# Performance work log

Measured on AMD Instinct MI355X. Metric: run time of the kernel, lower is better.

The kernel has to match this reference:

```python
import jax, jax.numpy as jnp
import numpy as np

EPS_MSG = 1e-7   # GENConv message epsilon
BN_EPS = 1e-5    # BatchNorm1d eps
NUM_GRAPHS = 1024


def _linear(x, W, b):
    return x @ W + b


def _batchnorm(x, gamma, beta):
    # training-mode batch statistics over the node dimension
    mu = jnp.mean(x, axis=0)
    var = jnp.mean((x - mu) ** 2, axis=0)
    return (x - mu) * jax.lax.rsqrt(var + BN_EPS) * gamma + beta


def _genconv(x, src, dst, e, t, W1, b1, gamma, beta, W2, b2, num_nodes):
    # message: relu(x_j + edge_attr) + eps, shape [E, H]
    msg = jax.nn.relu(x[src] + e) + EPS_MSG
    # learnable softmax aggregation over each destination's neighborhood
    s = msg * t
    m = jax.lax.stop_gradient(jax.ops.segment_max(s, dst, num_segments=num_nodes))
    m = jnp.where(jnp.isfinite(m), m, 0.0)
    ex = jnp.exp(s - m[dst])
    denom = jax.ops.segment_sum(ex, dst, num_segments=num_nodes)
    alpha = ex / (denom[dst] + 1e-16)
    agg = jax.ops.segment_sum(msg * alpha, dst, num_segments=num_nodes)  # [N, H]
    # GENConv MLP([H, 2H, H], norm='batch') applied to x + aggregated messages
    h = x + agg
    h = _linear(h, W1, b1)
    h = _batchnorm(h, gamma, beta)
    h = jax.nn.relu(h)
    return _linear(h, W2, b2)


def setup_inputs() -> dict:
    key = jax.random.key(0)
    N, E, FIN, FE, H, L, G, OUT = 50000, 1000000, 32, 16, 64, 4, NUM_GRAPHS, 1
    ks = jax.random.split(key, 32)

    def rn(k, shape, fan_in):
        return jax.random.normal(k, shape, dtype=jnp.float32) * (1.0 / np.sqrt(fan_in))

    inp = {}
    inp["x"] = jax.random.normal(ks[0], (N, FIN), dtype=jnp.float32)
    inp["edge_attr"] = jax.random.normal(ks[1], (E, FE), dtype=jnp.float32)
    inp["edge_index"] = jax.random.randint(ks[2], (2, E), 0, N)
    inp["batch"] = jnp.sort(jax.random.randint(ks[3], (N,), 0, G))
    # atom encoder: Linear(FIN,H) ReLU Linear(H,H) ReLU
    inp["atom_W1"] = rn(ks[4], (FIN, H), FIN); inp["atom_b1"] = jnp.zeros((H,), jnp.float32)
    inp["atom_W2"] = rn(ks[5], (H, H), H);     inp["atom_b2"] = jnp.zeros((H,), jnp.float32)
    # bond encoder: Linear(FE,H) ReLU Linear(H,H) ReLU
    inp["bond_W1"] = rn(ks[6], (FE, H), FE);   inp["bond_b1"] = jnp.zeros((H,), jnp.float32)
    inp["bond_W2"] = rn(ks[7], (H, H), H);     inp["bond_b2"] = jnp.zeros((H,), jnp.float32)
    # stacked GENConv params (L layers)
    inp["conv_t"] = jnp.ones((L,), jnp.float32)
    inp["conv_W1"] = rn(ks[8], (L, H, 2 * H), H)
    inp["conv_b1"] = jnp.zeros((L, 2 * H), jnp.float32)
    inp["conv_gamma"] = jnp.ones((L, 2 * H), jnp.float32)
    inp["conv_beta"] = jnp.zeros((L, 2 * H), jnp.float32)
    inp["conv_W2"] = rn(ks[9], (L, 2 * H, H), 2 * H)
    inp["conv_b2"] = jnp.zeros((L, H), jnp.float32)
    # head
    inp["lin1_W"] = rn(ks[10], (H, H), H);     inp["lin1_b"] = jnp.zeros((H,), jnp.float32)
    inp["lin2_W"] = rn(ks[11], (H, OUT), H);   inp["lin2_b"] = jnp.zeros((OUT,), jnp.float32)
    return inp


def reference(x, edge_attr, atom_W1, atom_b1, atom_W2, atom_b2,
              bond_W1, bond_b1, bond_W2, bond_b2,
              conv_t, conv_W1, conv_b1, conv_gamma, conv_beta, conv_W2, conv_b2,
              lin1_W, lin1_b, lin2_W, lin2_b,
              edge_index, batch):
    N = x.shape[0]
    src, dst = edge_index[0], edge_index[1]
    h = jax.nn.relu(_linear(jax.nn.relu(_linear(x, atom_W1, atom_b1)), atom_W2, atom_b2))
    e = jax.nn.relu(_linear(jax.nn.relu(_linear(edge_attr, bond_W1, bond_b1)), bond_W2, bond_b2))
    L = conv_t.shape[0]
    for i in range(L):
        h = _genconv(h, src, dst, e, conv_t[i], conv_W1[i], conv_b1[i],
                     conv_gamma[i], conv_beta[i], conv_W2[i], conv_b2[i], N)
        if i < L - 1:
            h = jax.nn.relu(h)
    g = jax.ops.segment_sum(h, batch, num_segments=NUM_GRAPHS)  # global_add_pool
    g = jax.nn.relu(_linear(g, lin1_W, lin1_b))
    return _linear(g, lin2_W, lin2_b)
```

## Files before the change

kernel.cpp:

```cpp
#include <hip/hip_runtime.h>
#include <hip/hip_bf16.h>
#include <math.h>

typedef __attribute__((ext_vector_type(8))) short bf16x8;
typedef __attribute__((ext_vector_type(4))) float f32x4;

__device__ inline unsigned f2bf(float f) {
    union { __hip_bfloat16 h; unsigned short u; } cv;
    cv.h = __float2bfloat16(f);
    return (unsigned)cv.u;
}
__device__ inline float bfu(unsigned u) {
    return __uint_as_float(u << 16);
}


__global__ void k_hist(const int* __restrict__ dst, int* __restrict__ counts, int E) {
    int e = blockIdx.x * blockDim.x + threadIdx.x;
    if (e < E) atomicAdd(&counts[dst[e]], 1);
}

__global__ void k_scan1(const int* __restrict__ counts, int* __restrict__ row_ptr,
                        int* __restrict__ csum, int n) {
    __shared__ int buf[1024];
    int tid = threadIdx.x;
    int base = blockIdx.x * 1024;
    int v = (base + tid < n) ? counts[base + tid] : 0;
    buf[tid] = v;
    __syncthreads();
    int inc = v;
    for (int off = 1; off < 1024; off <<= 1) {
        int add = (tid >= off) ? buf[tid - off] : 0;
        __syncthreads();
        inc += add;
        buf[tid] = inc;
        __syncthreads();
    }
    if (base + tid < n) row_ptr[base + tid] = inc - v;
    if (tid == 1023) csum[blockIdx.x] = inc;
}

__global__ void k_scan2(int* __restrict__ csum, int nc, int* __restrict__ total) {
    if (threadIdx.x == 0) {
        int run = 0;
        for (int i = 0; i < nc; ++i) { int c = csum[i]; csum[i] = run; run += c; }
        *total = run;
    }
}

__global__ void k_scan3(int* __restrict__ row_ptr, const int* __restrict__ csum,
                        const int* __restrict__ total, int n) {
    int i = blockIdx.x * blockDim.x + threadIdx.x;
    if (i < n) row_ptr[i] += csum[i >> 10];
    if (i == 0) row_ptr[n] = *total;
}

#define ECH 4096
__global__ __launch_bounds__(256) void k_scatter(const int* __restrict__ src,
                          const int* __restrict__ dst,
                          const int* __restrict__ row_ptr, int* __restrict__ fill,
                          int2* __restrict__ spe, int E, int NS) {
    int bs = blockIdx.x & 7;
    int chunk = blockIdx.x >> 3;
    int base = chunk * ECH;
    int lo = bs * NS, hi = lo + NS;
#pragma unroll 1
    for (int j = 0; j < ECH / 256; ++j) {
        int e = base + j * 256 + threadIdx.x;
        if (e < E) {
            int d = dst[e];
            if (d >= lo && d < hi) {
                int pos = row_ptr[d] + atomicAdd(&fill[d], 1);
                spe[pos] = make_int2(src[e], e);
            }
        }
    }
}

__global__ void k_gptr(const int* __restrict__ batch, int* __restrict__ gptr, int n, int G) {
    int i = blockIdx.x * blockDim.x + threadIdx.x;
    if (i > n) return;
    if (i == 0) {
        int b0 = batch[0];
        for (int g = 0; g <= b0; ++g) gptr[g] = 0;
    } else if (i == n) {
        int bl = batch[n - 1];
        for (int g = bl + 1; g <= G; ++g) gptr[g] = n;
    } else {
        int b = batch[i], pb = batch[i - 1];
        for (int g = pb + 1; g <= b; ++g) gptr[g] = i;
    }
}


__global__ void k_wt(const float* __restrict__ W1, const float* __restrict__ W2,
                     unsigned short* __restrict__ W1b, unsigned short* __restrict__ W2tb) {
    int tid = blockIdx.x * blockDim.x + threadIdx.x;
    if (tid < 1024) {
        int j = tid / 16, k = tid % 16;
        W1b[j * 16 + k] = (unsigned short)f2bf(W1[k * 64 + j]);
    }
    if (tid < 4096) {
        int j = tid / 64, k = tid % 64;
        W2tb[j * 64 + k] = (unsigned short)f2bf(W2[k * 64 + j]);
    }
}

__global__ void k_wtc(const float* __restrict__ W1, const float* __restrict__ W2,
                      unsigned short* __restrict__ W1tb, unsigned short* __restrict__ W2tb,
                      int L) {
    int idx = blockIdx.x * blockDim.x + threadIdx.x;
    int tot = L * 8192;
    if (idx < tot) {
        int l = idx / 8192, r = idx % 8192;
        int j = r / 64, k = r % 64;
        W1tb[(long)l * 8192 + j * 64 + k] = (unsigned short)f2bf(W1[(long)l * 8192 + k * 128 + j]);
        int j2 = r / 128, k2 = r % 128;
        W2tb[(long)l * 8192 + j2 * 128 + k2] =
            (unsigned short)f2bf(W2[(long)l * 8192 + k2 * 64 + j2]);
    }
}


#define TM 128
__global__ __launch_bounds__(256) void k_atom(const float* __restrict__ x,
        const float* __restrict__ W1, const float* __restrict__ b1,
        const float* __restrict__ W2, const float* __restrict__ b2,
        float* __restrict__ out, unsigned short* __restrict__ hb, int M) {
    __shared__ float sU[TM * 65];
    __shared__ float sW1[32 * 64];
    __shared__ float sW2[64 * 64];
    __shared__ float sB1[64], sB2[64];
#define A_IN(r, c) sU[(r) * 33 + (c)]
#define A_T1(r, c) sU[(r) * 65 + (c)]
    int tid = threadIdx.x;
    int base = blockIdx.x * TM;
    for (int i = tid; i < 32 * 64 / 4; i += 256) ((float4*)sW1)[i] = ((const float4*)W1)[i];
    for (int i = tid; i < 64 * 64 / 4; i += 256) ((float4*)sW2)[i] = ((const float4*)W2)[i];
    if (tid < 64) { sB1[tid] = b1[tid]; sB2[tid] = b2[tid]; }
    for (int i = tid; i < TM * 32 / 4; i += 256) {
        int r = i / 8, c4 = i % 8;
        int row = base + r;
        float4 v = (row < M) ? ((const float4*)(x + (long)row * 32))[c4] : make_float4(0, 0, 0, 0);
        A_IN(r, c4 * 4 + 0) = v.x; A_IN(r, c4 * 4 + 1) = v.y;
        A_IN(r, c4 * 4 + 2) = v.z; A_IN(r, c4 * 4 + 3) = v.w;
    }
    __syncthreads();
    int r0 = (tid / 16) * 8;
    int c0 = (tid % 16) * 4;
    float acc[8][4];
#pragma unroll
    for (int i = 0; i < 8; i++)
#pragma unroll
        for (int j = 0; j < 4; j++) acc[i][j] = sB1[c0 + j];
    for (int k = 0; k < 32; k++) {
        float a[8], b[4];
#pragma unroll
        for (int i = 0; i < 8; i++) a[i] = A_IN(r0 + i, k);
#pragma unroll
        for (int j = 0; j < 4; j++) b[j] = sW1[k * 64 + c0 + j];
#pragma unroll
        for (int i = 0; i < 8; i++)
#pragma unroll
            for (int j = 0; j < 4; j++) acc[i][j] += a[i] * b[j];
    }
    __syncthreads();
#pragma unroll
    for (int i = 0; i < 8; i++)
#pragma unroll
        for (int j = 0; j < 4; j++) A_T1(r0 + i, c0 + j) = fmaxf(acc[i][j], 0.f);
    __syncthreads();
#pragma unroll
    for (int i = 0; i < 8; i++)
#pragma unroll
        for (int j = 0; j < 4; j++) acc[i][j] = sB2[c0 + j];
    for (int k = 0; k < 64; k++) {
        float a[8], b[4];
#pragma unroll
        for (int i = 0; i < 8; i++) a[i] = A_T1(r0 + i, k);
#pragma unroll
        for (int j = 0; j < 4; j++) b[j] = sW2[k * 64 + c0 + j];
#pragma unroll
        for (int i = 0; i < 8; i++)
#pragma unroll
            for (int j = 0; j < 4; j++) acc[i][j] += a[i] * b[j];
    }
#pragma unroll
    for (int i = 0; i < 8; i++) {
        int row = base + r0 + i;
        if (row < M) {
            float4 v = make_float4(fmaxf(acc[i][0], 0.f), fmaxf(acc[i][1], 0.f),
                                   fmaxf(acc[i][2], 0.f), fmaxf(acc[i][3], 0.f));
            *(float4*)(out + (long)row * 64 + c0) = v;
            unsigned p01 = f2bf(v.x) | (f2bf(v.y) << 16);
            unsigned p23 = f2bf(v.z) | (f2bf(v.w) << 16);
            *(uint2*)(hb + (long)row * 64 + c0) = make_uint2(p01, p23);
        }
    }
}


__global__ __launch_bounds__(256) void k_bond(const float* __restrict__ ea,
        const int2* __restrict__ spe,
        const unsigned short* __restrict__ W1b, const float* __restrict__ b1,
        const unsigned short* __restrict__ W2tb, const float* __restrict__ b2,
        unsigned short* __restrict__ e_q, int E) {
    __shared__ unsigned sT1[128 * 32];
    __shared__ unsigned sW2[64 * 32];
    int tid = threadIdx.x;

    for (int i = tid; i < 2048; i += 256) {
        int rw = i >> 5, cp = i & 31;
        sW2[rw * 32 + (cp ^ ((rw & 7) << 2))] = ((const unsigned*)W2tb)[i];
    }

    int wv = tid >> 6, lane = tid & 63;
    int lr = lane & 15, q = lane >> 4;

    union { bf16x8 v; uint4 u4; } bf1[4];
    float bias1[4];
#pragma unroll
    for (int nt = 0; nt < 4; ++nt) {
        bf1[nt].u4 = make_uint4(0, 0, 0, 0);
        if (q < 2)
            bf1[nt].u4 = *(const uint4*)(W1b + (nt * 16 + lr) * 16 + q * 8);
        bias1[nt] = b1[nt * 16 + lr];
    }

#pragma unroll
    for (int mt1 = 0; mt1 < 2; ++mt1) {
        int rtile = wv * 2 + mt1;
        long row1 = (long)blockIdx.x * 128 + rtile * 16 + lr;
        long eidx = row1 < (long)E ? row1 : (long)(E - 1);
        int eid = spe[eidx].y;
        union { bf16x8 v; uint4 u4; unsigned u[4]; } af1;
        af1.u4 = make_uint4(0, 0, 0, 0);
        if (q < 2) {
            const float4* er = (const float4*)(ea + (long)eid * 16 + q * 8);
            float4 u0 = er[0], u1 = er[1];
            af1.u[0] = f2bf(u0.x) | (f2bf(u0.y) << 16);
            af1.u[1] = f2bf(u0.z) | (f2bf(u0.w) << 16);
            af1.u[2] = f2bf(u1.x) | (f2bf(u1.y) << 16);
            af1.u[3] = f2bf(u1.z) | (f2bf(u1.w) << 16);
        }
#pragma unroll
        for (int nt = 0; nt < 4; ++nt) {
            f32x4 c0;
            c0[0] = bias1[nt]; c0[1] = bias1[nt]; c0[2] = bias1[nt]; c0[3] = bias1[nt];
            f32x4 d = __builtin_amdgcn_mfma_f32_16x16x32_bf16(af1.v, bf1[nt].v, c0, 0, 0, 0);
#pragma unroll
            for (int i = 0; i < 4; ++i) {
                unsigned hv = f2bf(fmaxf(d[i], 0.f));
                unsigned ov = (unsigned)__shfl_xor((int)hv, 1, 64);
                if ((lr & 1) == 0) {
                    int r = rtile * 16 + q * 4 + i;
                    int cp = nt * 8 + (lr >> 1);
                    sT1[r * 32 + (cp ^ ((r & 7) << 2))] = hv | (ov << 16);
                }
            }
        }
    }
    __syncthreads();

    bf16x8 bf[4][2];
#pragma unroll
    for (int nt = 0; nt < 4; ++nt)
#pragma unroll
        for (int ks = 0; ks < 2; ++ks) {
            int rw = nt * 16 + lr;
            int u = rw * 32 + ((ks * 16 + q * 4) ^ ((rw & 7) << 2));
            bf[nt][ks] = *(const bf16x8*)&sW2[u];
        }
    f32x4 acc[2][4];
#pragma unroll
    for (int mt = 0; mt < 2; ++mt)
#pragma unroll
        for (int nt = 0; nt < 4; ++nt) {
            float bias = b2[nt * 16 + lr];
            f32x4 c0; c0[0] = bias; c0[1] = bias; c0[2] = bias; c0[3] = bias;
            acc[mt][nt] = c0;
        }
#pragma unroll
    for (int mt = 0; mt < 2; ++mt) {
        int rw = (wv * 2 + mt) * 16 + lr;
#pragma unroll
        for (int ks = 0; ks < 2; ++ks) {
            int u = rw * 32 + ((ks * 16 + q * 4) ^ ((rw & 7) << 2));
            bf16x8 af = *(const bf16x8*)&sT1[u];
#pragma unroll
            for (int nt = 0; nt < 4; ++nt)
                acc[mt][nt] = __builtin_amdgcn_mfma_f32_16x16x32_bf16(
                    af, bf[nt][ks], acc[mt][nt], 0, 0, 0);
        }
    }
#pragma unroll
    for (int mt = 0; mt < 2; ++mt)
#pragma unroll
        for (int nt = 0; nt < 4; ++nt) {
            long r0 = (long)blockIdx.x * 128 + (wv * 2 + mt) * 16 + q * 4;
            unsigned p01 = f2bf(fmaxf(acc[mt][nt][0], 0.f)) |
                           (f2bf(fmaxf(acc[mt][nt][1], 0.f)) << 16);
            unsigned p23 = f2bf(fmaxf(acc[mt][nt][2], 0.f)) |
                           (f2bf(fmaxf(acc[mt][nt][3], 0.f)) << 16);
            long qb = ((r0 >> 2) * 64 + nt * 16 + lr) * 4;
            if (r0 + 3 < (long)E) {
                *(uint2*)(e_q + qb) = make_uint2(p01, p23);
            } else {
                unsigned vv[4] = {p01 & 0xffff, p01 >> 16, p23 & 0xffff, p23 >> 16};
#pragma unroll
                for (int i = 0; i < 4; ++i)
                    if (r0 + i < (long)E) e_q[qb + i] = (unsigned short)vv[i];
            }
        }
}


__global__ __launch_bounds__(256) void k_agg(const float* __restrict__ h,
        const unsigned short* __restrict__ h_bf,
        const unsigned short* __restrict__ e_q, const int2* __restrict__ spe,
        const int* __restrict__ row_ptr, const float* __restrict__ t_ptr, int layer,
        unsigned short* __restrict__ yb, int n) {
    int wid = blockIdx.x * 4 + (threadIdx.x >> 6);
    int lane = threadIdx.x & 63;
    if (wid >= n) return;
    wid = __builtin_amdgcn_readfirstlane(wid);
    float tval = t_ptr[layer];
    int beg = row_ptr[wid], end = row_ptr[wid + 1];
    float m = -INFINITY, den = 0.f, num = 0.f;
    int i = beg;
    int astart = (beg + 3) & ~3; if (astart > end) astart = end;
    int aend = end & ~3;         if (aend < astart) aend = astart;
    for (; i < astart; ++i) {
        int s = spe[i].x;
        float ev = bfu((unsigned)e_q[((long)(i >> 2) * 64 + lane) * 4 + (i & 3)]);
        float hv = bfu((unsigned)h_bf[(long)s * 64 + lane]);
        float msg = fmaxf(hv + ev, 0.f) + 1e-7f;
        float sv = msg * tval;
        float mn = fmaxf(m, sv);
        float sc = __expf(m - mn);
        float w = __expf(sv - mn);
        den = den * sc + w;
        num = num * sc + w * msg;
        m = mn;
    }
    for (; i + 8 <= aend; i += 8) {
        int s0 = spe[i].x,     s1 = spe[i + 1].x, s2 = spe[i + 2].x, s3 = spe[i + 3].x;
        int s4 = spe[i + 4].x, s5 = spe[i + 5].x, s6 = spe[i + 6].x, s7 = spe[i + 7].x;
        uint2 ea0 = *(const uint2*)(e_q + ((long)(i >> 2) * 64 + lane) * 4);
        uint2 ea1 = *(const uint2*)(e_q + ((long)((i >> 2) + 1) * 64 + lane) * 4);
        float hv0 = bfu((unsigned)h_bf[(long)s0 * 64 + lane]);
        float hv1 = bfu((unsigned)h_bf[(long)s1 * 64 + lane]);
        float hv2 = bfu((unsigned)h_bf[(long)s2 * 64 + lane]);
        float hv3 = bfu((unsigned)h_bf[(long)s3 * 64 + lane]);
        float hv4 = bfu((unsigned)h_bf[(long)s4 * 64 + lane]);
        float hv5 = bfu((unsigned)h_bf[(long)s5 * 64 + lane]);
        float hv6 = bfu((unsigned)h_bf[(long)s6 * 64 + lane]);
        float hv7 = bfu((unsigned)h_bf[(long)s7 * 64 + lane]);
        float msg0 = fmaxf(hv0 + bfu(ea0.x & 0xffff), 0.f) + 1e-7f;
        float msg1 = fmaxf(hv1 + bfu(ea0.x >> 16), 0.f) + 1e-7f;
        float msg2 = fmaxf(hv2 + bfu(ea0.y & 0xffff), 0.f) + 1e-7f;
        float msg3 = fmaxf(hv3 + bfu(ea0.y >> 16), 0.f) + 1e-7f;
        float msg4 = fmaxf(hv4 + bfu(ea1.x & 0xffff), 0.f) + 1e-7f;
        float msg5 = fmaxf(hv5 + bfu(ea1.x >> 16), 0.f) + 1e-7f;
        float msg6 = fmaxf(hv6 + bfu(ea1.y & 0xffff), 0.f) + 1e-7f;
        float msg7 = fmaxf(hv7 + bfu(ea1.y >> 16), 0.f) + 1e-7f;
        float sv0 = msg0 * tval, sv1 = msg1 * tval, sv2 = msg2 * tval, sv3 = msg3 * tval;
        float sv4 = msg4 * tval, sv5 = msg5 * tval, sv6 = msg6 * tval, sv7 = msg7 * tval;
        float mn = fmaxf(fmaxf(fmaxf(fmaxf(m, sv0), fmaxf(sv1, sv2)),
                               fmaxf(fmaxf(sv3, sv4), fmaxf(sv5, sv6))), sv7);
        float sc = __expf(m - mn);
        float w0 = __expf(sv0 - mn), w1 = __expf(sv1 - mn);
        float w2 = __expf(sv2 - mn), w3 = __expf(sv3 - mn);
        float w4 = __expf(sv4 - mn), w5 = __expf(sv5 - mn);
        float w6 = __expf(sv6 - mn), w7 = __expf(sv7 - mn);
        den = den * sc + (((w0 + w1) + (w2 + w3)) + ((w4 + w5) + (w6 + w7)));
        num = num * sc + (((w0 * msg0 + w1 * msg1) + (w2 * msg2 + w3 * msg3)) +
                          ((w4 * msg4 + w5 * msg5) + (w6 * msg6 + w7 * msg7)));
        m = mn;
    }
    for (; i < aend; i += 4) {
        int s0 = spe[i].x, s1 = spe[i + 1].x, s2 = spe[i + 2].x, s3 = spe[i + 3].x;
        uint2 ee = *(const uint2*)(e_q + ((long)(i >> 2) * 64 + lane) * 4);
        float hv0 = bfu((unsigned)h_bf[(long)s0 * 64 + lane]);
        float hv1 = bfu((unsigned)h_bf[(long)s1 * 64 + lane]);
        float hv2 = bfu((unsigned)h_bf[(long)s2 * 64 + lane]);
        float hv3 = bfu((unsigned)h_bf[(long)s3 * 64 + lane]);
        float msg0 = fmaxf(hv0 + bfu(ee.x & 0xffff), 0.f) + 1e-7f;
        float msg1 = fmaxf(hv1 + bfu(ee.x >> 16), 0.f) + 1e-7f;
        float msg2 = fmaxf(hv2 + bfu(ee.y & 0xffff), 0.f) + 1e-7f;
        float msg3 = fmaxf(hv3 + bfu(ee.y >> 16), 0.f) + 1e-7f;
        float sv0 = msg0 * tval, sv1 = msg1 * tval;
        float sv2 = msg2 * tval, sv3 = msg3 * tval;
        float mn = fmaxf(fmaxf(fmaxf(m, sv0), fmaxf(sv1, sv2)), sv3);
        float sc = __expf(m - mn);
        float w0 = __expf(sv0 - mn);
        float w1 = __expf(sv1 - mn);
        float w2 = __expf(sv2 - mn);
        float w3 = __expf(sv3 - mn);
        den = den * sc + ((w0 + w1) + (w2 + w3));
        num = num * sc + ((w0 * msg0 + w1 * msg1) + (w2 * msg2 + w3 * msg3));
        m = mn;
    }
    for (; i < end; ++i) {
        int s = spe[i].x;
        float ev = bfu((unsigned)e_q[((long)(i >> 2) * 64 + lane) * 4 + (i & 3)]);
        float hv = bfu((unsigned)h_bf[(long)s * 64 + lane]);
        float msg = fmaxf(hv + ev, 0.f) + 1e-7f;
        float sv = msg * tval;
        float mn = fmaxf(m, sv);
        float sc = __expf(m - mn);
        float w = __expf(sv - mn);
        den = den * sc + w;
        num = num * sc + w * msg;
        m = mn;
    }
    float agg = (end > beg) ? num / (den + 1e-16f) : 0.f;
    yb[(long)wid * 64 + lane] = (unsigned short)f2bf(h[(long)wid * 64 + lane] + agg);
}


__global__ __launch_bounds__(256) void k_gemm1(const unsigned* __restrict__ yb,
        const unsigned* __restrict__ W1tb, const float* __restrict__ b1,
        unsigned* __restrict__ h1b, float* __restrict__ part, int n) {
    __shared__ unsigned sY[128 * 32];
    __shared__ unsigned sW[128 * 32];
    int tid = threadIdx.x;
    int base = blockIdx.x * 128;
    for (int i = tid; i < 4096; i += 256) {
        int rw = i >> 5, cp = i & 31;
        sW[rw * 32 + (cp ^ ((rw & 7) << 2))] = W1tb[i];
    }
#pragma unroll
    for (int j = 0; j < 16; ++j) {
        int u = j * 256 + tid;
        int r = u >> 5, cp = u & 31;
        long row = base + r;
        unsigned v = (row < (long)n) ? yb[row * 32 + cp] : 0u;
        sY[r * 32 + (cp ^ ((r & 7) << 2))] = v;
    }
    __syncthreads();
    int wv = tid >> 6, lane = tid & 63, lr = lane & 15, q = lane >> 4;
    bf16x8 bf[2][2];
    float bias[2];
#pragma unroll
    for (int nt2 = 0; nt2 < 2; ++nt2) {
        int rw = wv * 32 + nt2 * 16 + lr;
#pragma unroll
        for (int ks = 0; ks < 2; ++ks)
            bf[nt2][ks] = *(const bf16x8*)&sW[rw * 32 + ((ks * 16 + q * 4) ^ ((rw & 7) << 2))];
        bias[nt2] = b1[rw];
    }
    float ps[2] = {0, 0}, ps2[2] = {0, 0};
#pragma unroll 1
    for (int mt = 0; mt < 8; ++mt) {
        int ar = mt * 16 + lr;
        bf16x8 a0 = *(const bf16x8*)&sY[ar * 32 + ((q * 4) ^ ((ar & 7) << 2))];
        bf16x8 a1 = *(const bf16x8*)&sY[ar * 32 + ((16 + q * 4) ^ ((ar & 7) << 2))];
#pragma unroll
        for (int nt2 = 0; nt2 < 2; ++nt2) {
            f32x4 acc;
            acc[0] = bias[nt2]; acc[1] = bias[nt2]; acc[2] = bias[nt2]; acc[3] = bias[nt2];
            acc = __builtin_amdgcn_mfma_f32_16x16x32_bf16(a0, bf[nt2][0], acc, 0, 0, 0);
            acc = __builtin_amdgcn_mfma_f32_16x16x32_bf16(a1, bf[nt2][1], acc, 0, 0, 0);
            int col = wv * 32 + nt2 * 16 + lr;
#pragma unroll
            for (int i = 0; i < 4; ++i) {
                long row = base + mt * 16 + q * 4 + i;
                float v = acc[i];
                unsigned hv = f2bf(v);
                unsigned ov = (unsigned)__shfl_xor((int)hv, 1, 64);
                bool in = row < (long)n;
                if (in) { ps[nt2] += v; ps2[nt2] += v * v; }
                if (in && (lr & 1) == 0)
                    h1b[row * 64 + ((unsigned)col >> 1)] = hv | (ov << 16);
            }
        }
    }
#pragma unroll
    for (int nt2 = 0; nt2 < 2; ++nt2) {
        float s = ps[nt2], s2 = ps2[nt2];
        s += __shfl_down(s, 32, 64);  s += __shfl_down(s, 16, 64);
        s2 += __shfl_down(s2, 32, 64); s2 += __shfl_down(s2, 16, 64);
        if (lane < 16) {
            int col = wv * 32 + nt2 * 16 + lr;
            part[(long)blockIdx.x * 256 + col] = s;
            part[(long)blockIdx.x * 256 + 128 + col] = s2;
        }
    }
}


__global__ __launch_bounds__(256) void k_bnred(const float* __restrict__ part,
                                               float* __restrict__ part2, int nblk) {
    int c = threadIdx.x;
    int b = blockIdx.x;
    float s = 0.f;
    for (int r = b; r < nblk; r += 64) s += part[(long)r * 256 + c];
    part2[b * 256 + c] = s;
}

__global__ __launch_bounds__(1024) void k_bnfin(const float* __restrict__ part2,
                        const float* __restrict__ gamma, const float* __restrict__ beta,
                        float* __restrict__ scale, float* __restrict__ shift, float invN) {
    __shared__ float red[4][256];
    __shared__ float tot[256];
    int c = threadIdx.x & 255;
    int g = threadIdx.x >> 8;
    float s = 0.f;
#pragma unroll
    for (int r = 0; r < 16; ++r) s += part2[(g * 16 + r) * 256 + c];
    red[g][c] = s;
    __syncthreads();
    if (threadIdx.x < 256) tot[c] = red[0][c] + red[1][c] + red[2][c] + red[3][c];
    __syncthreads();
    if (threadIdx.x < 128) {
        int cc = threadIdx.x;
        float mu = tot[cc] * invN;
        float var = fmaxf(tot[128 + cc] * invN - mu * mu, 0.f);
        float sc = gamma[cc] * rsqrtf(var + 1e-5f);
        scale[cc] = sc;
        shift[cc] = beta[cc] - mu * sc;
    }
}


__global__ __launch_bounds__(256) void k_gemm2(const unsigned* __restrict__ h1b,
        const float* __restrict__ scale, const float* __restrict__ shift,
        const unsigned* __restrict__ W2tbL, const float* __restrict__ b2,
        float* __restrict__ hout, unsigned short* __restrict__ hb, int n, int dorelu) {
    __shared__ unsigned sA[128 * 64];
    __shared__ unsigned sW[64 * 64];
    __shared__ float sSc[128], sSh[128];
    int tid = threadIdx.x;
    int base = blockIdx.x * 128;
    if (tid < 128) { sSc[tid] = scale[tid]; sSh[tid] = shift[tid]; }
    for (int i = tid; i < 4096; i += 256) {
        int rw = i >> 6, cp = i & 63;
        sW[rw * 64 + (cp ^ ((rw & 7) << 2))] = W2tbL[i];
    }
    __syncthreads();
#pragma unroll
    for (int j = 0; j < 32; ++j) {
        int u = j * 256 + tid;
        int r = u >> 6, cp = u & 63;
        long row = base + r;
        unsigned w = 0;
        if (row < (long)n) {
            unsigned hv = h1b[row * 64 + cp];
            float v0 = fmaxf(bfu(hv & 0xffff) * sSc[2 * cp] + sSh[2 * cp], 0.f);
            float v1 = fmaxf(bfu(hv >> 16) * sSc[2 * cp + 1] + sSh[2 * cp + 1], 0.f);
            w = f2bf(v0) | (f2bf(v1) << 16);
        }
        sA[r * 64 + (cp ^ ((r & 7) << 2))] = w;
    }
    __syncthreads();
    int wv = tid >> 6, lane = tid & 63, lr = lane & 15, q = lane >> 4;
    bf16x8 bf[4];
    {
        int rw = wv * 16 + lr;
#pragma unroll
        for (int ks = 0; ks < 4; ++ks)
            bf[ks] = *(const bf16x8*)&sW[rw * 64 + ((ks * 16 + q * 4) ^ ((rw & 7) << 2))];
    }
    float bias = b2[wv * 16 + lr];
#pragma unroll 1
    for (int mt = 0; mt < 8; ++mt) {
        int ar = mt * 16 + lr;
        f32x4 acc;
        acc[0] = bias; acc[1] = bias; acc[2] = bias; acc[3] = bias;
#pragma unroll
        for (int ks = 0; ks < 4; ++ks) {
            bf16x8 a = *(const bf16x8*)&sA[ar * 64 + ((ks * 16 + q * 4) ^ ((ar & 7) << 2))];
            acc = __builtin_amdgcn_mfma_f32_16x16x32_bf16(a, bf[ks], acc, 0, 0, 0);
        }
        int col = wv * 16 + lr;
#pragma unroll
        for (int i = 0; i < 4; ++i) {
            long row = base + mt * 16 + q * 4 + i;
            float v = dorelu ? fmaxf(acc[i], 0.f) : acc[i];
            unsigned hv = f2bf(v);
            unsigned ov = (unsigned)__shfl_xor((int)hv, 1, 64);
            if (row < (long)n) {
                hout[row * 64 + col] = v;
                if (dorelu && (lr & 1) == 0)
                    *(unsigned*)(hb + row * 64 + (col & ~1)) = hv | (ov << 16);
            }
        }
    }
}


__global__ __launch_bounds__(64) void k_head(const float* __restrict__ h,
        const int* __restrict__ gptr,
        const float* __restrict__ W1, const float* __restrict__ b1,
        const float* __restrict__ W2, const float* __restrict__ b2,
        float* __restrict__ out) {
    int g = blockIdx.x;
    int lane = threadIdx.x;
    int beg = gptr[g], end = gptr[g + 1];
    float s = 0.f;
    for (int r = beg; r < end; ++r) s += h[(long)r * 64 + lane];
    __shared__ float sg[64];
    sg[lane] = s;
    __syncthreads();
    float acc = b1[lane];
    for (int k = 0; k < 64; k++) acc += sg[k] * W1[k * 64 + lane];
    acc = fmaxf(acc, 0.f);
    float v = acc * W2[lane];
#pragma unroll
    for (int off = 32; off > 0; off >>= 1) v += __shfl_down(v, off, 64);
    if (lane == 0) out[g] = v + b2[0];
}


extern "C" void kernel_launch(void* const* d_in, const int* in_sizes, int n_in,
                              void* d_out, int out_size, void* d_ws, size_t ws_size,
                              hipStream_t stream) {
    const float* x      = (const float*)d_in[0];
    const float* ea     = (const float*)d_in[1];
    const int*   ei     = (const int*)d_in[2];
    const int*   batch  = (const int*)d_in[3];
    const float* atomW1 = (const float*)d_in[4];
    const float* atomb1 = (const float*)d_in[5];
    const float* atomW2 = (const float*)d_in[6];
    const float* atomb2 = (const float*)d_in[7];
    const float* bondW1 = (const float*)d_in[8];
    const float* bondb1 = (const float*)d_in[9];
    const float* bondW2 = (const float*)d_in[10];
    const float* bondb2 = (const float*)d_in[11];
    const float* convT  = (const float*)d_in[12];
    const float* convW1 = (const float*)d_in[13];
    const float* convb1 = (const float*)d_in[14];
    const float* convG  = (const float*)d_in[15];
    const float* convBt = (const float*)d_in[16];
    const float* convW2 = (const float*)d_in[17];
    const float* convb2 = (const float*)d_in[18];
    const float* lin1W  = (const float*)d_in[19];
    const float* lin1b  = (const float*)d_in[20];
    const float* lin2W  = (const float*)d_in[21];
    const float* lin2b  = (const float*)d_in[22];
    float* out = (float*)d_out;

    const int N = in_sizes[0] / 32;
    const int E = in_sizes[1] / 16;
    const int G = out_size;
    const int Lconv = in_sizes[12];
    const int nchunk = (N + 1023) / 1024;
    const int nblk128 = (N + 127) / 128;
    const int NS = (N + 7) / 8;
    const int nchE = (E + ECH - 1) / ECH;
    const size_t nquad = (size_t)((E + 3) / 4);

    size_t need = 0;
    auto count = [&](size_t bytes) { need += (bytes + 255) & ~(size_t)255; };
    count(nquad * 4 * 64 * 2);
    count((size_t)N * 64 * 4);
    count((size_t)N * 64 * 2);
    count((size_t)N * 64 * 2);
    count((size_t)N * 128 * 2);
    count((size_t)E * 8);
    count((size_t)(N + 1) * 4);
    count((size_t)N * 4);
    count((size_t)N * 4);
    count((size_t)(G + 1) * 4);
    count((size_t)nblk128 * 256 * 4);
    count((size_t)64 * 256 * 4);
    count(128 * 4); count(128 * 4);
    count((size_t)(nchunk + 1) * 4);
    count(4);
    count(1024 * 2);
    count(4096 * 2);
    count((size_t)Lconv * 8192 * 2);
    count((size_t)Lconv * 8192 * 2);
    if (ws_size < need) {
        hipMemsetAsync(d_out, 0, (size_t)out_size * 4, stream);
        return;
    }

    char* ws = (char*)d_ws;
    size_t off = 0;
    auto alloc = [&](size_t bytes) -> void* {
        void* p = ws + off;
        off += (bytes + 255) & ~(size_t)255;
        return p;
    };
    unsigned short* e_q = (unsigned short*)alloc(nquad * 4 * 64 * 2);
    float* h_cur    = (float*)alloc((size_t)N * 64 * 4);
    unsigned short* h_bf = (unsigned short*)alloc((size_t)N * 64 * 2);
    unsigned short* y_bf = (unsigned short*)alloc((size_t)N * 64 * 2);
    unsigned short* h1b  = (unsigned short*)alloc((size_t)N * 128 * 2);
    int2*  spe      = (int2*)alloc((size_t)E * 8);
    int*   row_ptr  = (int*)alloc((size_t)(N + 1) * 4);
    int*   counts   = (int*)alloc((size_t)N * 4);
    int*   fill     = (int*)alloc((size_t)N * 4);
    int*   gptr     = (int*)alloc((size_t)(G + 1) * 4);
    float* part     = (float*)alloc((size_t)nblk128 * 256 * 4);
    float* part2    = (float*)alloc((size_t)64 * 256 * 4);
    float* bnscale  = (float*)alloc(128 * 4);
    float* bnshift  = (float*)alloc(128 * 4);
    int*   csum     = (int*)alloc((size_t)(nchunk + 1) * 4);
    int*   totalp   = (int*)alloc(4);
    unsigned short* W1b  = (unsigned short*)alloc(1024 * 2);
    unsigned short* W2tb = (unsigned short*)alloc(4096 * 2);
    unsigned short* cW1tb = (unsigned short*)alloc((size_t)Lconv * 8192 * 2);
    unsigned short* cW2tb = (unsigned short*)alloc((size_t)Lconv * 8192 * 2);
    (void)n_in;

    hipMemsetAsync(counts, 0, (size_t)N * 4, stream);
    hipMemsetAsync(fill, 0, (size_t)N * 4, stream);

    const int* src = ei;
    const int* dst = ei + E;

    k_hist<<<(E + 255) / 256, 256, 0, stream>>>(dst, counts, E);
    k_scan1<<<nchunk, 1024, 0, stream>>>(counts, row_ptr, csum, N);
    k_scan2<<<1, 64, 0, stream>>>(csum, nchunk, totalp);
    k_scan3<<<(N + 255) / 256, 256, 0, stream>>>(row_ptr, csum, totalp, N);
    k_scatter<<<nchE * 8, 256, 0, stream>>>(src, dst, row_ptr, fill, spe, E, NS);
    k_gptr<<<(N + 256) / 256, 256, 0, stream>>>(batch, gptr, N, G);
    k_wt<<<16, 256, 0, stream>>>(bondW1, bondW2, W1b, W2tb);
    k_wtc<<<(Lconv * 8192 + 255) / 256, 256, 0, stream>>>(convW1, convW2, cW1tb, cW2tb, Lconv);

    k_atom<<<(N + TM - 1) / TM, 256, 0, stream>>>(x, atomW1, atomb1, atomW2, atomb2,
                                                  h_cur, h_bf, N);
    k_bond<<<(E + 127) / 128, 256, 0, stream>>>(ea, spe, W1b, bondb1, W2tb, bondb2, e_q, E);

    for (int l = 0; l < Lconv; ++l) {
        k_agg<<<(N + 3) / 4, 256, 0, stream>>>(h_cur, h_bf, e_q, spe, row_ptr, convT, l,
                                               y_bf, N);
        k_gemm1<<<nblk128, 256, 0, stream>>>((const unsigned*)y_bf,
                                             (const unsigned*)(cW1tb + (size_t)l * 8192),
                                             convb1 + (size_t)l * 128,
                                             (unsigned*)h1b, part, N);
        k_bnred<<<64, 256, 0, stream>>>(part, part2, nblk128);
        k_bnfin<<<1, 1024, 0, stream>>>(part2, convG + (size_t)l * 128, convBt + (size_t)l * 128,
                                        bnscale, bnshift, 1.0f / (float)N);
        k_gemm2<<<nblk128, 256, 0, stream>>>((const unsigned*)h1b, bnscale, bnshift,
                                             (const unsigned*)(cW2tb + (size_t)l * 8192),
                                             convb2 + (size_t)l * 64, h_cur, h_bf, N,
                                             (l < Lconv - 1) ? 1 : 0);
    }

    k_head<<<G, 64, 0, stream>>>(h_cur, gptr, lin1W, lin1b, lin2W, lin2b, out);
}
```

Measured before the change: 535.1 us.

## Replace 8-pass CSR scatter with two-level bucket partition and swap MFMA operands in bond encoder

The CSR build previously scanned the whole edge list eight times, once per destination range. It now does a single pass that partitions edges into 64 destination buckets in a packed staging buffer, using block-local histograms and shared-memory atomics. A second kernel then scatters each bucket into its final CSR slots, so global atomics and writes stay within a localized range. Separately, the bond encoder's first MFMA has its operands swapped so each lane holds four consecutive columns for one row. Those can be packed straight into shared memory, which removes the shuffle and half-idle lanes. The cost is an extra E*8-byte staging buffer, one more kernel launch, and a packing scheme that needs src below 2^24 and a bucket size below 2^16.

```diff
diff --git a/kernel.cpp b/kernel.cpp
--- a/kernel.cpp
+++ b/kernel.cpp
@@ -55,25 +55,63 @@
     if (i == 0) row_ptr[n] = *total;
 }
 
-#define ECH 4096
-__global__ __launch_bounds__(256) void k_scatter(const int* __restrict__ src,
-                          const int* __restrict__ dst,
-                          const int* __restrict__ row_ptr, int* __restrict__ fill,
-                          int2* __restrict__ spe, int E, int NS) {
-    int bs = blockIdx.x & 7;
-    int chunk = blockIdx.x >> 3;
-    int base = chunk * ECH;
-    int lo = bs * NS, hi = lo + NS;
+
+#define ECH2 4096
+__global__ __launch_bounds__(256) void k_part(const int* __restrict__ src,
+        const int* __restrict__ dst, const int* __restrict__ row_ptr,
+        int* __restrict__ bfill, unsigned long long* __restrict__ staging,
+        int E, int NS64, int N) {
+    __shared__ int lh[64], lbase[64], lfill[64];
+    int tid = threadIdx.x;
+    if (tid < 64) lh[tid] = 0;
+    __syncthreads();
+    int base = blockIdx.x * ECH2;
 #pragma unroll 1
-    for (int j = 0; j < ECH / 256; ++j) {
-        int e = base + j * 256 + threadIdx.x;
+    for (int j = 0; j < ECH2 / 256; ++j) {
+        int e = base + j * 256 + tid;
+        if (e < E) atomicAdd(&lh[dst[e] / NS64], 1);
+    }
+    __syncthreads();
+    if (tid < 64) {
+        int bs = row_ptr[min(tid * NS64, N)];
+        lbase[tid] = bs + atomicAdd(&bfill[tid], lh[tid]);
+        lfill[tid] = 0;
+    }
+    __syncthreads();
+#pragma unroll 1
+    for (int j = 0; j < ECH2 / 256; ++j) {
+        int e = base + j * 256 + tid;
         if (e < E) {
             int d = dst[e];
-            if (d >= lo && d < hi) {
-                int pos = row_ptr[d] + atomicAdd(&fill[d], 1);
-                spe[pos] = make_int2(src[e], e);
-            }
-        }
+            int b = d / NS64;
+            int r = atomicAdd(&lfill[b], 1);
+            unsigned long long pk = (unsigned long long)((unsigned)src[e] & 0xffffffu)
+                | ((unsigned long long)((unsigned)(d - b * NS64) & 0xffffu) << 24)
+                | ((unsigned long long)(unsigned)e << 40);
+            staging[lbase[b] + r] = pk;
+        }
+    }
+}
+
+__global__ __launch_bounds__(256) void k_scat2(const unsigned long long* __restrict__ staging,
+        const int* __restrict__ row_ptr, int* __restrict__ fill,
+        int2* __restrict__ spe, int NS64, int N) {
+    int b = blockIdx.x >> 1;
+    int half = blockIdx.x & 1;
+    int s0 = row_ptr[min(b * NS64, N)];
+    int s1 = row_ptr[min((b + 1) * NS64, N)];
+    int cnt = s1 - s0;
+    int h0 = cnt >> 1;
+    int start = s0 + (half ? h0 : 0);
+    int len = half ? (cnt - h0) : h0;
+    for (int i = threadIdx.x; i < len; i += 256) {
+        unsigned long long pk = staging[start + i];
+        int srcv = (int)(pk & 0xffffffu);
+        int dloc = (int)((pk >> 24) & 0xffffu);
+        int eid  = (int)(pk >> 40);
+        int d = b * NS64 + dloc;
+        int pos = row_ptr[d] + atomicAdd(&fill[d], 1);
+        spe[pos] = make_int2(srcv, eid);
     }
 }
 
@@ -218,13 +256,13 @@
     int lr = lane & 15, q = lane >> 4;
 
     union { bf16x8 v; uint4 u4; } bf1[4];
-    float bias1[4];
+    float4 bias1[4];
 #pragma unroll
     for (int nt = 0; nt < 4; ++nt) {
         bf1[nt].u4 = make_uint4(0, 0, 0, 0);
         if (q < 2)
             bf1[nt].u4 = *(const uint4*)(W1b + (nt * 16 + lr) * 16 + q * 8);
-        bias1[nt] = b1[nt * 16 + lr];
+        bias1[nt] = *(const float4*)(b1 + nt * 16 + q * 4);
     }
 
 #pragma unroll
@@ -243,21 +281,18 @@
             af1.u[2] = f2bf(u1.x) | (f2bf(u1.y) << 16);
             af1.u[3] = f2bf(u1.z) | (f2bf(u1.w) << 16);
         }
+        int r = rtile * 16 + lr;
 #pragma unroll
         for (int nt = 0; nt < 4; ++nt) {
             f32x4 c0;
-            c0[0] = bias1[nt]; c0[1] = bias1[nt]; c0[2] = bias1[nt]; c0[3] = bias1[nt];
-            f32x4 d = __builtin_amdgcn_mfma_f32_16x16x32_bf16(af1.v, bf1[nt].v, c0, 0, 0, 0);
-#pragma unroll
-            for (int i = 0; i < 4; ++i) {
-                unsigned hv = f2bf(fmaxf(d[i], 0.f));
-                unsigned ov = (unsigned)__shfl_xor((int)hv, 1, 64);
-                if ((lr & 1) == 0) {
-                    int r = rtile * 16 + q * 4 + i;
-                    int cp = nt * 8 + (lr >> 1);
-                    sT1[r * 32 + (cp ^ ((r & 7) << 2))] = hv | (ov << 16);
-                }
-            }
+            c0[0] = bias1[nt].x; c0[1] = bias1[nt].y;
+            c0[2] = bias1[nt].z; c0[3] = bias1[nt].w;
+            f32x4 d = __builtin_amdgcn_mfma_f32_16x16x32_bf16(bf1[nt].v, af1.v, c0, 0, 0, 0);
+            unsigned p01 = f2bf(fmaxf(d[0], 0.f)) | (f2bf(fmaxf(d[1], 0.f)) << 16);
+            unsigned p23 = f2bf(fmaxf(d[2], 0.f)) | (f2bf(fmaxf(d[3], 0.f)) << 16);
+            int cp = nt * 8 + q * 2;
+            sT1[r * 32 + (cp ^ ((r & 7) << 2))] = p01;
+            sT1[r * 32 + ((cp + 1) ^ ((r & 7) << 2))] = p23;
         }
     }
     __syncthreads();
@@ -647,8 +682,8 @@
     const int Lconv = in_sizes[12];
     const int nchunk = (N + 1023) / 1024;
     const int nblk128 = (N + 127) / 128;
-    const int NS = (N + 7) / 8;
-    const int nchE = (E + ECH - 1) / ECH;
+    const int NS64 = (N + 63) / 64;
+    const int nchE2 = (E + ECH2 - 1) / ECH2;
     const size_t nquad = (size_t)((E + 3) / 4);
 
     size_t need = 0;
@@ -659,9 +694,11 @@
     count((size_t)N * 64 * 2);
     count((size_t)N * 128 * 2);
     count((size_t)E * 8);
+    count((size_t)E * 8);
     count((size_t)(N + 1) * 4);
     count((size_t)N * 4);
     count((size_t)N * 4);
+    count(256);
     count((size_t)(G + 1) * 4);
     count((size_t)nblk128 * 256 * 4);
     count((size_t)64 * 256 * 4);
@@ -690,9 +727,11 @@
     unsigned short* y_bf = (unsigned short*)alloc((size_t)N * 64 * 2);
     unsigned short* h1b  = (unsigned short*)alloc((size_t)N * 128 * 2);
     int2*  spe      = (int2*)alloc((size_t)E * 8);
+    unsigned long long* staging = (unsigned long long*)alloc((size_t)E * 8);
     int*   row_ptr  = (int*)alloc((size_t)(N + 1) * 4);
     int*   counts   = (int*)alloc((size_t)N * 4);
     int*   fill     = (int*)alloc((size_t)N * 4);
+    int*   bfill    = (int*)alloc(256);
     int*   gptr     = (int*)alloc((size_t)(G + 1) * 4);
     float* part     = (float*)alloc((size_t)nblk128 * 256 * 4);
     float* part2    = (float*)alloc((size_t)64 * 256 * 4);
@@ -708,6 +747,7 @@
 
     hipMemsetAsync(counts, 0, (size_t)N * 4, stream);
     hipMemsetAsync(fill, 0, (size_t)N * 4, stream);
+    hipMemsetAsync(bfill, 0, 256, stream);
 
     const int* src = ei;
     const int* dst = ei + E;
@@ -716,7 +756,8 @@
     k_scan1<<<nchunk, 1024, 0, stream>>>(counts, row_ptr, csum, N);
     k_scan2<<<1, 64, 0, stream>>>(csum, nchunk, totalp);
     k_scan3<<<(N + 255) / 256, 256, 0, stream>>>(row_ptr, csum, totalp, N);
-    k_scatter<<<nchE * 8, 256, 0, stream>>>(src, dst, row_ptr, fill, spe, E, NS);
+    k_part<<<nchE2, 256, 0, stream>>>(src, dst, row_ptr, bfill, staging, E, NS64, N);
+    k_scat2<<<128, 256, 0, stream>>>(staging, row_ptr, fill, spe, NS64, N);
     k_gptr<<<(N + 256) / 256, 256, 0, stream>>>(batch, gptr, N, G);
     k_wt<<<16, 256, 0, stream>>>(bondW1, bondW2, W1b, W2tb);
     k_wtc<<<(Lconv * 8192 + 255) / 256, 256, 0, stream>>>(convW1, convW2, cW1tb, cW2tb, Lconv);
```

Result: no change. 536.9 us (+0.3%).
